# Kernel tuning notes

Hardware: AMD Instinct MI355X
Metric: run time of the kernel (lower is better)

Reference implementation:

```python
import jax, jax.numpy as jnp
import numpy as np

B, N, T, M, D, H = 2, 2048, 8, 256, 1024, 16
HD = D // H
EPS = 1e-5


def setup_inputs() -> dict:
    key = jax.random.key(0)
    ks = jax.random.split(key, 12)
    text_tokens = jax.random.normal(ks[0], (B, N, D), dtype=jnp.float32)
    media = jax.random.normal(ks[1], (B, T, M, D), dtype=jnp.float32)
    # exactly T media markers, evenly spaced, first at position 0 so no
    # fully-masked softmax row (matches well-formed usage of the module)
    loc = np.zeros((B, N), dtype=bool)
    loc[:, (np.arange(T) * (N // T))] = True
    media_locations = jnp.asarray(loc)
    s = 0.02
    return {
        "text_tokens": text_tokens,
        "media": media,
        "media_locations": media_locations,
        "ln_gamma": jnp.ones((D,), jnp.float32),
        "ln_beta": jnp.zeros((D,), jnp.float32),
        "wq": jax.random.normal(ks[2], (D, D), jnp.float32) * s,
        "wk": jax.random.normal(ks[3], (D, D), jnp.float32) * s,
        "wv": jax.random.normal(ks[4], (D, D), jnp.float32) * s,
        "bq": jnp.zeros((D,), jnp.float32),
        "bk": jnp.zeros((D,), jnp.float32),
        "bv": jnp.zeros((D,), jnp.float32),
        "w_out": jax.random.normal(ks[5], (D, D), jnp.float32) * s,
        "b_out": jnp.zeros((D,), jnp.float32),
    }


def _layernorm(x, gamma, beta):
    mu = jnp.mean(x, axis=-1, keepdims=True)
    var = jnp.mean(jnp.square(x - mu), axis=-1, keepdims=True)
    return (x - mu) * jax.lax.rsqrt(var + EPS) * gamma + beta


def reference(text_tokens, media, media_locations, ln_gamma, ln_beta,
              wq, wk, wv, bq, bk, bv, w_out, b_out):
    b, t, m, d = media.shape
    n = text_tokens.shape[1]
    h, hd = H, HD

    x = _layernorm(text_tokens, ln_gamma, ln_beta)          # [b,n,d]
    kv = media.reshape(b, t * m, d)                          # [b,tm,d]

    q = (x @ wq + bq).reshape(b, n, h, hd)
    k = (kv @ wk + bk).reshape(b, t * m, h, hd)
    v = (kv @ wv + bv).reshape(b, t * m, h, hd)

    scale = 1.0 / jnp.sqrt(jnp.asarray(hd, jnp.float32))
    scores = jnp.einsum('bnhk,bshk->bhns', q, k) * scale     # [b,h,n,tm]

    # media-locality mask: text token attends only to its immediately
    # preceding media frame (cumsum of media_locations == frame index)
    text_cumsum = jnp.cumsum(media_locations.astype(jnp.int32), axis=-1)  # [b,n]
    media_nums = jnp.repeat(jnp.arange(1, t + 1, dtype=jnp.int32), m)     # [tm]
    allowed = text_cumsum[:, :, None] == media_nums[None, None, :]        # [b,n,tm]
    scores = jnp.where(allowed[:, None, :, :], scores, -jnp.inf)

    attn = jax.nn.softmax(scores, axis=-1)                   # [b,h,n,tm]
    out = jnp.einsum('bhns,bshk->bnhk', attn, v).reshape(b, n, d)
    return out @ w_out + b_out
```

## Files before the change

kernel.cpp:

```cpp
#include <hip/hip_runtime.h>
#include <hip/hip_fp16.h>


typedef _Float16 h8 __attribute__((ext_vector_type(8)));
typedef _Float16 h4 __attribute__((ext_vector_type(4)));
typedef float f4 __attribute__((ext_vector_type(4)));

#define DI __device__ __forceinline__

DI void gload16(const void* g, void* l) {
  __builtin_amdgcn_global_load_lds((const __attribute__((address_space(1))) unsigned int*)g,
                                   (__attribute__((address_space(3))) unsigned int*)l, 16, 0, 0);
}

__global__ __launch_bounds__(256) void prep_kernel(
    const float* __restrict__ x, const float* __restrict__ gamma, const float* __restrict__ beta,
    _Float16* __restrict__ xh,
    const float* __restrict__ media, _Float16* __restrict__ kvh,
    const float* __restrict__ W0, const float* __restrict__ W1,
    const float* __restrict__ W2, const float* __restrict__ W3, _Float16* __restrict__ Wt,
    const int* __restrict__ locs, int* __restrict__ cnt, int* __restrict__ qlist) {
  int bid = blockIdx.x;
  int tid = threadIdx.x;
  if (bid < 4096) {
    int row = bid;
    const f4* xr = (const f4*)(x + (size_t)row * 1024);
    f4 v = xr[tid];
    float s = v[0] + v[1] + v[2] + v[3];
    float ss = v[0]*v[0] + v[1]*v[1] + v[2]*v[2] + v[3]*v[3];
    #pragma unroll
    for (int m = 1; m < 64; m <<= 1) { s += __shfl_xor(s, m); ss += __shfl_xor(ss, m); }
    __shared__ float red[8];
    int wid = tid >> 6, lane = tid & 63;
    if (lane == 0) { red[wid] = s; red[4 + wid] = ss; }
    __syncthreads();
    s = red[0] + red[1] + red[2] + red[3];
    ss = red[4] + red[5] + red[6] + red[7];
    float mean = s * (1.0f / 1024.0f);
    float var = ss * (1.0f / 1024.0f) - mean * mean;
    float rs = rsqrtf(var + 1e-5f);
    f4 g = ((const f4*)gamma)[tid], be = ((const f4*)beta)[tid];
    h4 o;
    #pragma unroll
    for (int j = 0; j < 4; ++j) o[j] = (_Float16)((v[j] - mean) * rs * g[j] + be[j]);
    ((h4*)(xh + (size_t)row * 1024))[tid] = o;
  } else if (bid < 8192) {
    int i = (bid - 4096) * 256 + tid;
    f4 v = ((const f4*)media)[i];
    h4 o;
    #pragma unroll
    for (int j = 0; j < 4; ++j) o[j] = (_Float16)v[j];
    ((h4*)kvh)[i] = o;
  } else if (bid < 12288) {
    int sec = bid - 8192;
    int z = sec >> 10, r = sec & 1023;
    const float* W = z == 0 ? W0 : z == 1 ? W1 : z == 2 ? W2 : W3;
    _Float16* out = Wt + (size_t)z * 1024 * 1024;
    __shared__ float tile[32][33];
    int i0 = (r & 31) * 32, o0 = (r >> 5) * 32;
    int tx = tid & 31, ty = tid >> 5;
    #pragma unroll
    for (int rr = 0; rr < 4; ++rr)
      tile[ty + rr * 8][tx] = W[(size_t)(i0 + ty + rr * 8) * 1024 + o0 + tx];
    __syncthreads();
    #pragma unroll
    for (int rr = 0; rr < 4; ++rr)
      out[(size_t)(o0 + ty + rr * 8) * 1024 + i0 + tx] = (_Float16)tile[tx][ty + rr * 8];
  } else {
    int b = bid - 12288;
    __shared__ int lcnt[8];
    if (tid < 8) lcnt[tid] = 0;
    __syncthreads();
    if (tid < 64) {
      int lane = tid;
      int run = 0; int v[32];
      #pragma unroll
      for (int i = 0; i < 32; ++i) { run += locs[b * 2048 + lane * 32 + i]; v[i] = run; }
      int incl = run;
      #pragma unroll
      for (int d = 1; d < 64; d <<= 1) { int t = __shfl_up(incl, d); if (lane >= d) incl += t; }
      int excl = incl - run;
      #pragma unroll
      for (int i = 0; i < 32; ++i) {
        int c = excl + v[i];
        if (c >= 1 && c <= 8) {
          int pos = atomicAdd(&lcnt[c - 1], 1);
          qlist[(b * 8 + (c - 1)) * 2048 + pos] = lane * 32 + i;
        }
      }
    }
    __syncthreads();
    if (tid < 8) cnt[b * 8 + tid] = lcnt[tid];
  }
}

struct GemmDesc { const _Float16* A; const _Float16* Bt; const float* bias; void* C; int mode; };
struct GemmBatch { GemmDesc d[3]; };

__global__ __launch_bounds__(512) void gemm128(GemmBatch gb) {
  GemmDesc g = gb.d[blockIdx.z];
  int row0 = blockIdx.y * 128, col0 = blockIdx.x * 128;
  __shared__ alignas(16) _Float16 As[128 * 64];
  __shared__ alignas(16) _Float16 Bs[128 * 64];
  int tid = threadIdx.x, lane = tid & 63, wid = tid >> 6;
  int wr = wid >> 2, wc = wid & 3;
  f4 acc[4][2] = {};
  int r0s = tid >> 3, c0s = tid & 7;
  int cg0 = c0s ^ (r0s & 7);
  int r1s = r0s + 64;
  int cg1 = c0s ^ (r1s & 7);
  const _Float16* gA0 = g.A + (size_t)(row0 + r0s) * 1024 + cg0 * 8;
  const _Float16* gA1 = g.A + (size_t)(row0 + r1s) * 1024 + cg1 * 8;
  const _Float16* gB0 = g.Bt + (size_t)(col0 + r0s) * 1024 + cg0 * 8;
  const _Float16* gB1 = g.Bt + (size_t)(col0 + r1s) * 1024 + cg1 * 8;
  #pragma unroll 1
  for (int kt = 0; kt < 16; ++kt) {
    __syncthreads();
    gload16(gA0 + kt * 64, (void*)&As[wid * 512]);
    gload16(gA1 + kt * 64, (void*)&As[4096 + wid * 512]);
    gload16(gB0 + kt * 64, (void*)&Bs[wid * 512]);
    gload16(gB1 + kt * 64, (void*)&Bs[4096 + wid * 512]);
    __syncthreads();
    h8 af[2][4], bf[2][2];
    #pragma unroll
    for (int kk = 0; kk < 2; ++kk) {
      #pragma unroll
      for (int m = 0; m < 4; ++m) {
        int r = wr * 64 + m * 16 + (lane & 15);
        int c = ((lane >> 4) + kk * 4) ^ (r & 7);
        af[kk][m] = *(const h8*)&As[r * 64 + c * 8];
      }
      #pragma unroll
      for (int n = 0; n < 2; ++n) {
        int r = wc * 32 + n * 16 + (lane & 15);
        int c = ((lane >> 4) + kk * 4) ^ (r & 7);
        bf[kk][n] = *(const h8*)&Bs[r * 64 + c * 8];
      }
    }
    #pragma unroll
    for (int kk = 0; kk < 2; ++kk)
      #pragma unroll
      for (int m = 0; m < 4; ++m)
        #pragma unroll
        for (int n = 0; n < 2; ++n)
          acc[m][n] = __builtin_amdgcn_mfma_f32_16x16x32_f16(af[kk][m], bf[kk][n], acc[m][n], 0, 0, 0);
  }
  int colb = col0 + wc * 32;
  float bias_v[2];
  #pragma unroll
  for (int n = 0; n < 2; ++n) bias_v[n] = g.bias[colb + n * 16 + (lane & 15)];
  #pragma unroll
  for (int m = 0; m < 4; ++m) {
    int row = row0 + wr * 64 + m * 16 + (lane >> 4) * 4;
    #pragma unroll
    for (int n = 0; n < 2; ++n) {
      int col = colb + n * 16 + (lane & 15);
      if (g.mode == 0) {
        _Float16* C = (_Float16*)g.C;
        #pragma unroll
        for (int j = 0; j < 4; ++j)
          C[(size_t)(row + j) * 1024 + col] = (_Float16)(acc[m][n][j] + bias_v[n]);
      } else if (g.mode == 1) {
        float* C = (float*)g.C;
        #pragma unroll
        for (int j = 0; j < 4; ++j)
          C[(size_t)(row + j) * 1024 + col] = acc[m][n][j] + bias_v[n];
      } else {
        _Float16* C = (_Float16*)g.C;
        h4 pk;
        #pragma unroll
        for (int j = 0; j < 4; ++j) pk[j] = (_Float16)(acc[m][n][j] + bias_v[n]);
        size_t vrow = (size_t)((row >> 11) * 1024 + col);
        *(h4*)&C[vrow * 2048 + (row & 2047)] = pk;
      }
    }
  }
}

__global__ __launch_bounds__(512) void attn_kernel(const _Float16* __restrict__ Qg,
    const _Float16* __restrict__ Kg, const _Float16* __restrict__ Vtg,
    const int* __restrict__ cnt, const int* __restrict__ qlist, _Float16* __restrict__ Og) {
  int h = blockIdx.x, f = blockIdx.y, b = blockIdx.z;
  __shared__ alignas(16) _Float16 Kl[256 * 64];
  __shared__ alignas(16) _Float16 Vl[64 * 256];
  __shared__ alignas(16) _Float16 Sl[8 * 16 * 256];
  int tid = threadIdx.x;
  for (int idx = tid; idx < 2048; idx += 512) {
    int r = idx >> 3, c = idx & 7;
    h8 v = *(const h8*)&Kg[((size_t)(b * 2048 + f * 256 + r)) * 1024 + h * 64 + c * 8];
    *(h8*)&Kl[r * 64 + ((c ^ (r & 7)) * 8)] = v;
  }
  for (int idx = tid; idx < 2048; idx += 512) {
    int d = idx >> 5, cc = idx & 31;
    h8 v = *(const h8*)&Vtg[((size_t)(b * 1024 + h * 64 + d)) * 2048 + f * 256 + cc * 8];
    *(h8*)&Vl[d * 256 + ((cc ^ (d & 7)) * 8)] = v;
  }
  __syncthreads();
  int nq = cnt[b * 8 + f];
  int lane = tid & 63, wid = tid >> 6;
  const int* ql = qlist + (b * 8 + f) * 2048;
  _Float16* Sw = &Sl[wid * 4096];
  for (int st = wid; st * 16 < nq; st += 8) {
    int qbase = st * 16;
    int nv = nq - qbase; if (nv > 16) nv = 16;
    int li = lane & 15; if (li > nv - 1) li = nv - 1;
    int qrow = b * 2048 + ql[qbase + li];
    h8 aq0 = *(const h8*)&Qg[(size_t)qrow * 1024 + h * 64 + (lane >> 4) * 8];
    h8 aq1 = *(const h8*)&Qg[(size_t)qrow * 1024 + h * 64 + 32 + (lane >> 4) * 8];
    f4 s[16];
    #pragma unroll
    for (int kt = 0; kt < 16; ++kt) {
      int key = kt * 16 + (lane & 15);
      int cb0 = lane >> 4;
      h8 bk0 = *(const h8*)&Kl[key * 64 + ((cb0 ^ (key & 7)) * 8)];
      h8 bk1 = *(const h8*)&Kl[key * 64 + (((cb0 + 4) ^ (key & 7)) * 8)];
      f4 z = {0.f, 0.f, 0.f, 0.f};
      s[kt] = __builtin_amdgcn_mfma_f32_16x16x32_f16(aq0, bk0, z, 0, 0, 0);
      s[kt] = __builtin_amdgcn_mfma_f32_16x16x32_f16(aq1, bk1, s[kt], 0, 0, 0);
    }
    float mx[4], sm[4];
    #pragma unroll
    for (int j = 0; j < 4; ++j) {
      float m = s[0][j];
      #pragma unroll
      for (int kt = 1; kt < 16; ++kt) m = fmaxf(m, s[kt][j]);
      #pragma unroll
      for (int d = 1; d < 16; d <<= 1) m = fmaxf(m, __shfl_xor(m, d));
      mx[j] = m; sm[j] = 0.f;
    }
    #pragma unroll
    for (int kt = 0; kt < 16; ++kt) {
      int keyb = kt * 16 + (lane & 15);
      int cbk = keyb >> 3, wi = keyb & 7;
      #pragma unroll
      for (int j = 0; j < 4; ++j) {
        float p = __expf((s[kt][j] - mx[j]) * 0.125f);
        sm[j] += p;
        int q = (lane >> 4) * 4 + j;
        Sw[q * 256 + ((cbk ^ (q & 7)) * 8) + wi] = (_Float16)p;
      }
    }
    #pragma unroll
    for (int j = 0; j < 4; ++j) {
      float x = sm[j];
      #pragma unroll
      for (int d = 1; d < 16; d <<= 1) x += __shfl_xor(x, d);
      sm[j] = x;
    }
    f4 o[4] = {};
    #pragma unroll
    for (int c32 = 0; c32 < 8; ++c32) {
      int qa = lane & 15;
      int cba = c32 * 4 + (lane >> 4);
      h8 pa = *(const h8*)&Sw[qa * 256 + ((cba ^ (qa & 7)) * 8)];
      #pragma unroll
      for (int dt = 0; dt < 4; ++dt) {
        int dd = dt * 16 + (lane & 15);
        h8 bv_ = *(const h8*)&Vl[dd * 256 + ((cba ^ (dd & 7)) * 8)];
        o[dt] = __builtin_amdgcn_mfma_f32_16x16x32_f16(pa, bv_, o[dt], 0, 0, 0);
      }
    }
    #pragma unroll
    for (int j = 0; j < 4; ++j) {
      int q = (lane >> 4) * 4 + j;
      if (q < nv) {
        int qr = __shfl(qrow, q);
        float inv = 1.0f / sm[j];
        #pragma unroll
        for (int dt = 0; dt < 4; ++dt)
          Og[(size_t)qr * 1024 + h * 64 + dt * 16 + (lane & 15)] = (_Float16)(o[dt][j] * inv);
      }
    }
  }
}

extern "C" void kernel_launch(void* const* d_in, const int* in_sizes, int n_in,
                              void* d_out, int out_size, void* d_ws, size_t ws_size,
                              hipStream_t stream) {
  const float* text  = (const float*)d_in[0];
  const float* media = (const float*)d_in[1];
  const int*   locs  = (const int*)d_in[2];
  const float* gamma = (const float*)d_in[3];
  const float* beta  = (const float*)d_in[4];
  const float* wq = (const float*)d_in[5];
  const float* wk = (const float*)d_in[6];
  const float* wv = (const float*)d_in[7];
  const float* bq = (const float*)d_in[8];
  const float* bk = (const float*)d_in[9];
  const float* bv = (const float*)d_in[10];
  const float* wo = (const float*)d_in[11];
  const float* bo = (const float*)d_in[12];

  char* ws = (char*)d_ws;
  size_t off = 0;
  auto take = [&](size_t bytes) { void* p = ws + off; off += (bytes + 255) & ~(size_t)255; return p; };
  _Float16* xh  = (_Float16*)take((size_t)4096 * 1024 * 2);
  _Float16* kvh = (_Float16*)take((size_t)4096 * 1024 * 2);
  _Float16* wt  = (_Float16*)take((size_t)4 * 1024 * 1024 * 2);
  _Float16* Qm  = (_Float16*)take((size_t)4096 * 1024 * 2);
  _Float16* Km  = (_Float16*)take((size_t)4096 * 1024 * 2);
  _Float16* Vt  = (_Float16*)take((size_t)2048 * 2048 * 2);
  _Float16* Om  = (_Float16*)take((size_t)4096 * 1024 * 2);
  int* cnt   = (int*)take(64 * sizeof(int));
  int* qlist = (int*)take((size_t)2 * 8 * 2048 * sizeof(int));

  prep_kernel<<<12290, 256, 0, stream>>>(text, gamma, beta, xh, media, kvh,
                                         wq, wk, wv, wo, wt, locs, cnt, qlist);

  GemmBatch gb;
  gb.d[0] = { xh,  wt,                       bq, (void*)Qm, 0 };
  gb.d[1] = { kvh, wt + (size_t)1 * 1048576, bk, (void*)Km, 0 };
  gb.d[2] = { kvh, wt + (size_t)2 * 1048576, bv, (void*)Vt, 2 };
  gemm128<<<dim3(8, 32, 3), 512, 0, stream>>>(gb);

  attn_kernel<<<dim3(16, 8, 2), 512, 0, stream>>>(Qm, Km, Vt, cnt, qlist, Om);

  GemmBatch gf;
  gf.d[0] = { Om, wt + (size_t)3 * 1048576, bo, d_out, 1 };
  gf.d[1] = gf.d[0];
  gf.d[2] = gf.d[0];
  gemm128<<<dim3(8, 32, 1), 512, 0, stream>>>(gf);
}
```

Before: 192.5 us.

## Use 256x256 double-buffered GEMM tile for the QKV projections

Adds a gemm256 kernel with 256x256 output tiles, double-buffered LDS staging through global_load_lds, and s_setprio around the MFMA block, and uses it for the batched Q/K/V projection. Larger tiles raise arithmetic intensity and cut global reloads of A and B. Prefetching the next k-tile while computing the current one is meant to hide load latency. The cost is only 192 blocks (4x16x3) for a GPU with many CUs, which lowers occupancy and parallelism, and each block holds 128 KB of LDS and 128 accumulator registers per lane.

After: 189.3 us. Within noise of the previous version (-1.7%).

```diff
diff --git a/kernel.cpp b/kernel.cpp
--- a/kernel.cpp
+++ b/kernel.cpp
@@ -12,6 +12,8 @@
   __builtin_amdgcn_global_load_lds((const __attribute__((address_space(1))) unsigned int*)g,
                                    (__attribute__((address_space(3))) unsigned int*)l, 16, 0, 0);
 }
+
+#define BAR() do { asm volatile("" ::: "memory"); __builtin_amdgcn_s_barrier(); asm volatile("" ::: "memory"); } while (0)
 
 __global__ __launch_bounds__(256) void prep_kernel(
     const float* __restrict__ x, const float* __restrict__ gamma, const float* __restrict__ beta,
@@ -96,6 +98,92 @@
 
 struct GemmDesc { const _Float16* A; const _Float16* Bt; const float* bias; void* C; int mode; };
 struct GemmBatch { GemmDesc d[3]; };
+
+__global__ __launch_bounds__(512, 2) void gemm256(GemmBatch gb) {
+  GemmDesc g = gb.d[blockIdx.z];
+  int row0 = blockIdx.y * 256, col0 = blockIdx.x * 256;
+  __shared__ alignas(16) _Float16 As[2][256 * 64];
+  __shared__ alignas(16) _Float16 Bs[2][256 * 64];
+  int tid = threadIdx.x, lane = tid & 63, wid = tid >> 6;
+  int wr = wid >> 2, wc = wid & 3;
+  int rs = tid >> 3;
+  int cg = (tid & 7) ^ (rs & 7);
+  const _Float16* gA = g.A + (size_t)(row0 + rs) * 1024 + cg * 8;
+  const _Float16* gB = g.Bt + (size_t)(col0 + rs) * 1024 + cg * 8;
+  int dstoff = wid * 8 * 64;
+  f4 acc[8][4] = {};
+
+  auto STAGE = [&](int kt, int buf) {
+    #pragma unroll
+    for (int s = 0; s < 4; ++s) {
+      gload16(gA + (size_t)s * 65536 + kt * 64, (void*)&As[buf][s * 4096 + dstoff]);
+      gload16(gB + (size_t)s * 65536 + kt * 64, (void*)&Bs[buf][s * 4096 + dstoff]);
+    }
+  };
+  STAGE(0, 0);
+  int c0 = (lane >> 4) ^ (lane & 7);
+  int c1 = (4 + (lane >> 4)) ^ (lane & 7);
+  #pragma unroll 1
+  for (int t = 0; t < 16; ++t) {
+    int buf = t & 1;
+    BAR();
+    if (t < 15) {
+      STAGE(t + 1, buf ^ 1);
+      asm volatile("s_waitcnt vmcnt(8)" ::: "memory");
+    } else {
+      asm volatile("s_waitcnt vmcnt(0)" ::: "memory");
+    }
+    BAR();
+    #pragma unroll
+    for (int kk = 0; kk < 2; ++kk) {
+      int cc = kk ? c1 : c0;
+      h8 a[8], b[4];
+      #pragma unroll
+      for (int m = 0; m < 8; ++m)
+        a[m] = *(const h8*)&As[buf][(wr * 128 + m * 16 + (lane & 15)) * 64 + cc * 8];
+      #pragma unroll
+      for (int n = 0; n < 4; ++n)
+        b[n] = *(const h8*)&Bs[buf][(wc * 64 + n * 16 + (lane & 15)) * 64 + cc * 8];
+      __builtin_amdgcn_s_setprio(1);
+      #pragma unroll
+      for (int m = 0; m < 8; ++m)
+        #pragma unroll
+        for (int n = 0; n < 4; ++n)
+          acc[m][n] = __builtin_amdgcn_mfma_f32_16x16x32_f16(a[m], b[n], acc[m][n], 0, 0, 0);
+      __builtin_amdgcn_s_setprio(0);
+    }
+  }
+  int colb = col0 + wc * 64;
+  float bias_v[4];
+  #pragma unroll
+  for (int n = 0; n < 4; ++n) bias_v[n] = g.bias[colb + n * 16 + (lane & 15)];
+  #pragma unroll
+  for (int m = 0; m < 8; ++m) {
+    int row = row0 + wr * 128 + m * 16 + (lane >> 4) * 4;
+    #pragma unroll
+    for (int n = 0; n < 4; ++n) {
+      int col = colb + n * 16 + (lane & 15);
+      if (g.mode == 0) {
+        _Float16* C = (_Float16*)g.C;
+        #pragma unroll
+        for (int j = 0; j < 4; ++j)
+          C[(size_t)(row + j) * 1024 + col] = (_Float16)(acc[m][n][j] + bias_v[n]);
+      } else if (g.mode == 1) {
+        float* C = (float*)g.C;
+        #pragma unroll
+        for (int j = 0; j < 4; ++j)
+          C[(size_t)(row + j) * 1024 + col] = acc[m][n][j] + bias_v[n];
+      } else {
+        _Float16* C = (_Float16*)g.C;
+        h4 pk;
+        #pragma unroll
+        for (int j = 0; j < 4; ++j) pk[j] = (_Float16)(acc[m][n][j] + bias_v[n]);
+        size_t vrow = (size_t)((row >> 11) * 1024 + col);
+        *(h4*)&C[vrow * 2048 + (row & 2047)] = pk;
+      }
+    }
+  }
+}
 
 __global__ __launch_bounds__(512) void gemm128(GemmBatch gb) {
   GemmDesc g = gb.d[blockIdx.z];
@@ -311,7 +399,7 @@
   gb.d[0] = { xh,  wt,                       bq, (void*)Qm, 0 };
   gb.d[1] = { kvh, wt + (size_t)1 * 1048576, bk, (void*)Km, 0 };
   gb.d[2] = { kvh, wt + (size_t)2 * 1048576, bv, (void*)Vt, 2 };
-  gemm128<<<dim3(8, 32, 3), 512, 0, stream>>>(gb);
+  gemm256<<<dim3(4, 16, 3), 512, 0, stream>>>(gb);
 
   attn_kernel<<<dim3(16, 8, 2), 512, 0, stream>>>(Qm, Km, Vt, cnt, qlist, Om);
 
```

## Widen weight transpose tiles, remap GEMM block order, add smaller-tile output GEMM

Applied to the files above, without the earlier changes.

The weight transpose now uses 64x64 tiles with float4 loads and 8-wide half stores, cutting the block count and improving store width. Both GEMMs remap block indices so consecutive blocks share the same column tile of B, which should improve L2 reuse. The output projection moves to a dedicated 64x128-tile kernel with 512 blocks, doubling block count to fill more CUs on the single-GEMM launch. The 64x65 float LDS tile may have bank conflicts on the column reads, and the smaller output tiles lower per-block data reuse.

New measurement: 173.1 us. -10.0%, faster.

```diff
diff --git a/kernel.cpp b/kernel.cpp
--- a/kernel.cpp
+++ b/kernel.cpp
@@ -51,23 +51,31 @@
     #pragma unroll
     for (int j = 0; j < 4; ++j) o[j] = (_Float16)v[j];
     ((h4*)kvh)[i] = o;
-  } else if (bid < 12288) {
+  } else if (bid < 9216) {
     int sec = bid - 8192;
-    int z = sec >> 10, r = sec & 1023;
+    int z = sec >> 8, r = sec & 255;
     const float* W = z == 0 ? W0 : z == 1 ? W1 : z == 2 ? W2 : W3;
     _Float16* out = Wt + (size_t)z * 1024 * 1024;
-    __shared__ float tile[32][33];
-    int i0 = (r & 31) * 32, o0 = (r >> 5) * 32;
-    int tx = tid & 31, ty = tid >> 5;
-    #pragma unroll
-    for (int rr = 0; rr < 4; ++rr)
-      tile[ty + rr * 8][tx] = W[(size_t)(i0 + ty + rr * 8) * 1024 + o0 + tx];
-    __syncthreads();
-    #pragma unroll
-    for (int rr = 0; rr < 4; ++rr)
-      out[(size_t)(o0 + ty + rr * 8) * 1024 + i0 + tx] = (_Float16)tile[tx][ty + rr * 8];
+    __shared__ float tileF[64][65];
+    int i0 = (r & 15) * 64, o0 = (r >> 4) * 64;
+    #pragma unroll
+    for (int p = 0; p < 4; ++p) {
+      int ir = p * 16 + (tid >> 4);
+      f4 v = *(const f4*)&W[(size_t)(i0 + ir) * 1024 + o0 + (tid & 15) * 4];
+      #pragma unroll
+      for (int j = 0; j < 4; ++j) tileF[ir][(tid & 15) * 4 + j] = v[j];
+    }
+    __syncthreads();
+    #pragma unroll
+    for (int p = 0; p < 2; ++p) {
+      int orow = p * 32 + (tid >> 3);
+      h8 v;
+      #pragma unroll
+      for (int j = 0; j < 8; ++j) v[j] = (_Float16)tileF[(tid & 7) * 8 + j][orow];
+      *(h8*)&out[(size_t)(o0 + orow) * 1024 + i0 + (tid & 7) * 8] = v;
+    }
   } else {
-    int b = bid - 12288;
+    int b = bid - 9216;
     __shared__ int lcnt[8];
     if (tid < 8) lcnt[tid] = 0;
     __syncthreads();
@@ -99,7 +107,9 @@
 
 __global__ __launch_bounds__(512) void gemm128(GemmBatch gb) {
   GemmDesc g = gb.d[blockIdx.z];
-  int row0 = blockIdx.y * 128, col0 = blockIdx.x * 128;
+  int id = blockIdx.y * 8 + blockIdx.x;
+  int id2 = (id & 7) * 32 + (id >> 3);
+  int row0 = (id2 >> 3) * 128, col0 = (id2 & 7) * 128;
   __shared__ alignas(16) _Float16 As[128 * 64];
   __shared__ alignas(16) _Float16 Bs[128 * 64];
   int tid = threadIdx.x, lane = tid & 63, wid = tid >> 6;
@@ -107,12 +117,10 @@
   f4 acc[4][2] = {};
   int r0s = tid >> 3, c0s = tid & 7;
   int cg0 = c0s ^ (r0s & 7);
-  int r1s = r0s + 64;
-  int cg1 = c0s ^ (r1s & 7);
   const _Float16* gA0 = g.A + (size_t)(row0 + r0s) * 1024 + cg0 * 8;
-  const _Float16* gA1 = g.A + (size_t)(row0 + r1s) * 1024 + cg1 * 8;
+  const _Float16* gA1 = gA0 + (size_t)64 * 1024;
   const _Float16* gB0 = g.Bt + (size_t)(col0 + r0s) * 1024 + cg0 * 8;
-  const _Float16* gB1 = g.Bt + (size_t)(col0 + r1s) * 1024 + cg1 * 8;
+  const _Float16* gB1 = gB0 + (size_t)64 * 1024;
   #pragma unroll 1
   for (int kt = 0; kt < 16; ++kt) {
     __syncthreads();
@@ -160,11 +168,6 @@
         #pragma unroll
         for (int j = 0; j < 4; ++j)
           C[(size_t)(row + j) * 1024 + col] = (_Float16)(acc[m][n][j] + bias_v[n]);
-      } else if (g.mode == 1) {
-        float* C = (float*)g.C;
-        #pragma unroll
-        for (int j = 0; j < 4; ++j)
-          C[(size_t)(row + j) * 1024 + col] = acc[m][n][j] + bias_v[n];
       } else {
         _Float16* C = (_Float16*)g.C;
         h4 pk;
@@ -173,6 +176,67 @@
         size_t vrow = (size_t)((row >> 11) * 1024 + col);
         *(h4*)&C[vrow * 2048 + (row & 2047)] = pk;
       }
+    }
+  }
+}
+
+__global__ __launch_bounds__(512) void gemm_out(const _Float16* __restrict__ A,
+    const _Float16* __restrict__ Bt, const float* __restrict__ bias, float* __restrict__ C) {
+  int id = blockIdx.y * 8 + blockIdx.x;
+  int id2 = (id & 7) * 64 + (id >> 3);
+  int row0 = (id2 >> 3) * 64, col0 = (id2 & 7) * 128;
+  __shared__ alignas(16) _Float16 As[64 * 64];
+  __shared__ alignas(16) _Float16 Bs[128 * 64];
+  int tid = threadIdx.x, lane = tid & 63, wid = tid >> 6;
+  int wr = wid >> 2, wc = wid & 3;
+  f4 acc[2][2] = {};
+  int rs = tid >> 3, c0s = tid & 7;
+  int cg = c0s ^ (rs & 7);
+  const _Float16* gA  = A  + (size_t)(row0 + rs) * 1024 + cg * 8;
+  const _Float16* gB0 = Bt + (size_t)(col0 + rs) * 1024 + cg * 8;
+  const _Float16* gB1 = gB0 + (size_t)64 * 1024;
+  #pragma unroll 1
+  for (int kt = 0; kt < 16; ++kt) {
+    __syncthreads();
+    gload16(gA  + kt * 64, (void*)&As[wid * 512]);
+    gload16(gB0 + kt * 64, (void*)&Bs[wid * 512]);
+    gload16(gB1 + kt * 64, (void*)&Bs[4096 + wid * 512]);
+    __syncthreads();
+    #pragma unroll
+    for (int kk = 0; kk < 2; ++kk) {
+      h8 a[2], b[2];
+      #pragma unroll
+      for (int m = 0; m < 2; ++m) {
+        int r = wr * 32 + m * 16 + (lane & 15);
+        int c = ((lane >> 4) + kk * 4) ^ (r & 7);
+        a[m] = *(const h8*)&As[r * 64 + c * 8];
+      }
+      #pragma unroll
+      for (int n = 0; n < 2; ++n) {
+        int r = wc * 32 + n * 16 + (lane & 15);
+        int c = ((lane >> 4) + kk * 4) ^ (r & 7);
+        b[n] = *(const h8*)&Bs[r * 64 + c * 8];
+      }
+      #pragma unroll
+      for (int m = 0; m < 2; ++m)
+        #pragma unroll
+        for (int n = 0; n < 2; ++n)
+          acc[m][n] = __builtin_amdgcn_mfma_f32_16x16x32_f16(a[m], b[n], acc[m][n], 0, 0, 0);
+    }
+  }
+  int colb = col0 + wc * 32;
+  float bias_v[2];
+  #pragma unroll
+  for (int n = 0; n < 2; ++n) bias_v[n] = bias[colb + n * 16 + (lane & 15)];
+  #pragma unroll
+  for (int m = 0; m < 2; ++m) {
+    int row = row0 + wr * 32 + m * 16 + (lane >> 4) * 4;
+    #pragma unroll
+    for (int n = 0; n < 2; ++n) {
+      int col = colb + n * 16 + (lane & 15);
+      #pragma unroll
+      for (int j = 0; j < 4; ++j)
+        C[(size_t)(row + j) * 1024 + col] = acc[m][n][j] + bias_v[n];
     }
   }
 }
@@ -304,8 +368,8 @@
   int* cnt   = (int*)take(64 * sizeof(int));
   int* qlist = (int*)take((size_t)2 * 8 * 2048 * sizeof(int));
 
-  prep_kernel<<<12290, 256, 0, stream>>>(text, gamma, beta, xh, media, kvh,
-                                         wq, wk, wv, wo, wt, locs, cnt, qlist);
+  prep_kernel<<<9218, 256, 0, stream>>>(text, gamma, beta, xh, media, kvh,
+                                        wq, wk, wv, wo, wt, locs, cnt, qlist);
 
   GemmBatch gb;
   gb.d[0] = { xh,  wt,                       bq, (void*)Qm, 0 };
@@ -315,9 +379,5 @@
 
   attn_kernel<<<dim3(16, 8, 2), 512, 0, stream>>>(Qm, Km, Vt, cnt, qlist, Om);
 
-  GemmBatch gf;
-  gf.d[0] = { Om, wt + (size_t)3 * 1048576, bo, d_out, 1 };
-  gf.d[1] = gf.d[0];
-  gf.d[2] = gf.d[0];
-  gemm128<<<dim3(8, 32, 1), 512, 0, stream>>>(gf);
-}
+  gemm_out<<<dim3(8, 64), 512, 0, stream>>>(Om, wt + (size_t)3 * 1048576, bo, (float*)d_out);
+}
```
